# Optimization experiments

Measured on AMD Instinct MI355X. Metric: run time of the kernel, lower is better.

Reference implementation:

```python
import jax, jax.numpy as jnp
import numpy as np

B, D, DOUT, R, H = 16384, 1024, 1024, 8, 16
DH = D // 2  # route hidden dim


def setup_inputs() -> dict:
    key = jax.random.key(0)
    ks = jax.random.split(key, 12)
    s = 0.02
    return {
        "x": jax.random.normal(ks[0], (B, D), dtype=jnp.float32),
        # nn.MultiheadAttention packed in_proj: [3D, D] (q,k,v stacked)
        "in_proj_w": jax.random.normal(ks[1], (3 * D, D), dtype=jnp.float32) * s,
        "in_proj_b": jax.random.normal(ks[2], (3 * D,), dtype=jnp.float32) * s,
        "out_proj_w": jax.random.normal(ks[3], (D, D), dtype=jnp.float32) * s,
        "out_proj_b": jax.random.normal(ks[4], (D,), dtype=jnp.float32) * s,
        # R expert MLPs, batched: Linear(D, D//2) -> ReLU -> Linear(D//2, DOUT)
        "W1": jax.random.normal(ks[5], (R, DH, D), dtype=jnp.float32) * s,
        "b1": jax.random.normal(ks[6], (R, DH), dtype=jnp.float32) * s,
        "W2": jax.random.normal(ks[7], (R, DOUT, DH), dtype=jnp.float32) * s,
        "b2": jax.random.normal(ks[8], (R, DOUT), dtype=jnp.float32) * s,
        # gate: Linear(D, R) + softmax
        "Wg": jax.random.normal(ks[9], (R, D), dtype=jnp.float32) * s,
        "bg": jax.random.normal(ks[10], (R,), dtype=jnp.float32) * s,
    }


def reference(x, in_proj_w, in_proj_b, out_proj_w, out_proj_b, W1, b1, W2, b2, Wg, bg):
    # --- MultiheadAttention over seq_len == 1 ---
    # softmax over a single key position is exactly 1 (for every head),
    # so attn_output == V; the Q/K projections provably do not affect the
    # output or any gradient (d softmax(single logit) = 0). Hence only the
    # V slice of the packed in_proj and the output projection matter.
    Wv = in_proj_w[2 * D:]          # [D, D]
    bv = in_proj_b[2 * D:]          # [D]
    v = x @ Wv.T + bv               # [B, D]
    attended = v @ out_proj_w.T + out_proj_b  # [B, D]

    # --- R small expert MLPs as one batched/grouped GEMM (dropout in eval mode = identity) ---
    h = jax.nn.relu(jnp.einsum('bd,rhd->brh', attended, W1) + b1)   # [B, R, DH]
    route_out = jnp.einsum('brh,roh->bro', h, W2) + b2              # [B, R, DOUT]

    # --- softmax gate over routes, computed from the ORIGINAL x ---
    gate = jax.nn.softmax(x @ Wg.T + bg, axis=-1)                   # [B, R]

    # gate-weighted sum over routes
    return jnp.einsum('bro,br->bo', route_out, gate)                # [B, DOUT]
```

## Files before the change

kernel.cpp:

```cpp
#include <hip/hip_runtime.h>
#include <hip/hip_bf16.h>
#include <cstdint>

typedef __hip_bfloat16 bf16;
typedef __attribute__((ext_vector_type(8))) short bfrag;
typedef __attribute__((ext_vector_type(4))) float facc;

#define B_    16384
#define D_    1024
#define DOUT_ 1024
#define R_    8
#define DH_   512
#define RH_   4096

#define BM 256
#define BN 256
#define BK 64

#define NXCD 8

#define AS1(p) ((const __attribute__((address_space(1))) void*)(p))
#define AS3(p) ((__attribute__((address_space(3))) void*)(p))

#define DSR(dst, addr, off) \
    asm volatile("ds_read_b128 %0, %1 offset:%c2" : "=v"(dst) : "v"(addr), "i"(off))
#define LGKM(n) do { asm volatile("s_waitcnt lgkmcnt(" #n ")" ::: "memory"); \
                     __builtin_amdgcn_sched_barrier(0); } while (0)

static __device__ __forceinline__ uint32_t pack2bf(float a, float b) {
    unsigned short ua = __builtin_bit_cast(unsigned short, __float2bfloat16(a));
    unsigned short ub = __builtin_bit_cast(unsigned short, __float2bfloat16(b));
    return (uint32_t)ua | ((uint32_t)ub << 16);
}

__global__ void k_cvt(const float* __restrict__ in, bf16* __restrict__ out, long n)
{
    long i = ((long)blockIdx.x * blockDim.x + threadIdx.x) * 4;
    if (i >= n) return;
    float4 v = *reinterpret_cast<const float4*>(in + i);
    uint2 o;
    o.x = pack2bf(v.x, v.y);
    o.y = pack2bf(v.z, v.w);
    *reinterpret_cast<uint2*>(out + i) = o;
}

__global__ void k_cvt_w2(const float* __restrict__ W2, bf16* __restrict__ out)
{
    int b = blockIdx.x;
    int r = b >> 10;
    int o = b & 1023;
    const float4* src = reinterpret_cast<const float4*>(W2 + ((long)r * DOUT_ + o) * DH_);
    bf16* dst = out + (long)o * RH_ + r * DH_;
    int t = threadIdx.x;
    float4 v = src[t];
    uint2 p;
    p.x = pack2bf(v.x, v.y);
    p.y = pack2bf(v.z, v.w);
    *reinterpret_cast<uint2*>(dst + t * 4) = p;
}

__global__ __launch_bounds__(256) void k_cvt_wvT(const float* __restrict__ Wv,
                                                 bf16* __restrict__ outT)
{
    __shared__ float tile[64][65];
    const int j0 = blockIdx.y * 64;
    const int d0 = blockIdx.x * 64;
    const int tx = threadIdx.x & 15;
    const int ty = threadIdx.x >> 4;
    #pragma unroll
    for (int p = 0; p < 4; ++p) {
        int r = p * 16 + ty;
        float4 v = *reinterpret_cast<const float4*>(&Wv[(long)(j0 + r) * D_ + d0 + tx * 4]);
        tile[r][tx * 4 + 0] = v.x; tile[r][tx * 4 + 1] = v.y;
        tile[r][tx * 4 + 2] = v.z; tile[r][tx * 4 + 3] = v.w;
    }
    __syncthreads();
    #pragma unroll
    for (int p = 0; p < 4; ++p) {
        int r = p * 16 + ty;
        uint2 o;
        o.x = pack2bf(tile[tx * 4 + 0][r], tile[tx * 4 + 1][r]);
        o.y = pack2bf(tile[tx * 4 + 2][r], tile[tx * 4 + 3][r]);
        *reinterpret_cast<uint2*>(&outT[(long)(d0 + r) * D_ + j0 + tx * 4]) = o;
    }
}

__global__ __launch_bounds__(256) void k_beff(const float* __restrict__ Wout,
                                              const float* __restrict__ bv,
                                              const float* __restrict__ bout,
                                              float* __restrict__ beff)
{
    const int o = blockIdx.x;
    float s = 0.f;
    for (int d = threadIdx.x; d < D_; d += 256)
        s += Wout[(long)o * D_ + d] * bv[d];
    #pragma unroll
    for (int off = 32; off > 0; off >>= 1) s += __shfl_xor(s, off);
    __shared__ float ps[4];
    if ((threadIdx.x & 63) == 0) ps[threadIdx.x >> 6] = s;
    __syncthreads();
    if (threadIdx.x == 0)
        beff[o] = ps[0] + ps[1] + ps[2] + ps[3] + bout[o];
}

__global__ __launch_bounds__(256) void k_gate(const float* __restrict__ x,
                                              const float* __restrict__ Wg,
                                              const float* __restrict__ bg,
                                              float* __restrict__ gate)
{
    __shared__ float sWg[R_ * D_];
    __shared__ float sbg[R_];
    for (int i = threadIdx.x; i < R_ * D_ / 4; i += 256)
        reinterpret_cast<float4*>(sWg)[i] = reinterpret_cast<const float4*>(Wg)[i];
    if (threadIdx.x < R_) sbg[threadIdx.x] = bg[threadIdx.x];
    __syncthreads();

    const int lane = threadIdx.x & 63;
    const int wave = threadIdx.x >> 6;
    const int row  = blockIdx.x * 4 + wave;

    const float4* xr = reinterpret_cast<const float4*>(x + (long)row * D_);
    float s[R_] = {};
    #pragma unroll
    for (int c = 0; c < 4; ++c) {
        float4 xv = xr[lane + c * 64];
        #pragma unroll
        for (int r = 0; r < R_; ++r) {
            float4 wv = reinterpret_cast<const float4*>(sWg + r * D_)[lane + c * 64];
            s[r] += xv.x * wv.x + xv.y * wv.y + xv.z * wv.z + xv.w * wv.w;
        }
    }
    #pragma unroll
    for (int r = 0; r < R_; ++r) {
        float v = s[r];
        #pragma unroll
        for (int off = 32; off > 0; off >>= 1) v += __shfl_xor(v, off);
        s[r] = v + sbg[r];
    }
    float m = s[0];
    #pragma unroll
    for (int r = 1; r < R_; ++r) m = fmaxf(m, s[r]);
    float den = 0.f;
    #pragma unroll
    for (int r = 0; r < R_; ++r) { s[r] = __expf(s[r] - m); den += s[r]; }
    float inv = 1.f / den;
    if (lane < R_) gate[(long)row * R_ + lane] = s[lane] * inv;
}

#define MFMA_BF16 __builtin_amdgcn_mfma_f32_16x16x32_bf16

template <int EPI>
__global__ __launch_bounds__(512, 2)
void k_gemm(const bf16* __restrict__ A, const bf16* __restrict__ Bm,
            const float* __restrict__ bias, const float* __restrict__ gate,
            const float* __restrict__ b2v, void* __restrict__ Cout,
            int M, int N, int K, int gate_row0)
{
    __shared__ char lds[131072];

    const int tid  = threadIdx.x;
    const int lane = tid & 63;
    const int wave = tid >> 6;
    const int wr   = wave >> 2;
    const int wc   = wave & 3;

    const int nwg  = gridDim.x * gridDim.y;
    const int orig = blockIdx.y * gridDim.x + blockIdx.x;
    const int xcd  = orig % NXCD;
    const int q    = nwg / NXCD;
    const int rr   = nwg % NXCD;
    const int wgid = (xcd < rr ? xcd * (q + 1) : rr * (q + 1) + (xcd - rr) * q)
                   + orig / NXCD;
    const int bn0  = (wgid % gridDim.x) * BN;
    const int bm0  = (wgid / gridDim.x) * BM;

    const int lrow = lane & 15;
    const int kgrp = lane >> 4;

    const int s_colb  = ((tid & 7) * 16) ^ (((tid >> 3) & 7) << 4);
    const int s_row   = tid >> 3;
    const int lds_off = tid * 16;

    const long Kb   = (long)K * 2;
    const long r64  = 64 * Kb;
    const long r128 = 128 * Kb;
    const char* gA0 = (const char*)A  + (long)(bm0 + s_row) * Kb + s_colb;
    const char* gB0 = (const char*)Bm + (long)(bn0 + s_row) * Kb + s_colb;

    auto stageH = [&](int buf, int h, long kb) {
        char* ldst = lds + buf * 65536
                   + (h < 2 ? h * 16384 : 32768 + (h - 2) * 16384) + lds_off;
        const char* g = (h < 2 ? gA0 + h * r128 : gB0 + (h - 2) * r128) + kb;
        __builtin_amdgcn_global_load_lds(AS1(g),       AS3(ldst),        16, 0, 0);
        __builtin_amdgcn_global_load_lds(AS1(g + r64), AS3(ldst + 8192), 16, 0, 0);
    };

    const int swzk  = (lrow & 7) << 4;
    const int colK0 = (kgrp * 16) ^ swzk;
    const int colK1 = (kgrp * 16 + 64) ^ swzk;
    const uint32_t ldsbase = (uint32_t)(uintptr_t)AS3(lds);
    const uint32_t aA00 = ldsbase + (wr * 128 + lrow) * 128 + colK0;
    const uint32_t aA01 = ldsbase + (wr * 128 + lrow) * 128 + colK1;
    const uint32_t aB00 = ldsbase + 32768 + (wc * 64 + lrow) * 128 + colK0;
    const uint32_t aB01 = ldsbase + 32768 + (wc * 64 + lrow) * 128 + colK1;
    const uint32_t aA10 = aA00 + 65536, aA11 = aA01 + 65536;
    const uint32_t aB10 = aB00 + 65536, aB11 = aB01 + 65536;

    facc acc[8][4];
    #pragma unroll
    for (int m = 0; m < 8; ++m)
        #pragma unroll
        for (int n = 0; n < 4; ++n)
            acc[m][n] = facc{0.f, 0.f, 0.f, 0.f};

    const int NT = K / BK;

    bfrag aF[4][2];
    bfrag bHi[2][2];
    bfrag bLoE[2][2];
    bfrag bLoO[2][2];

    auto rdQ0 = [&](bfrag (&bLo)[2][2], uint32_t A0, uint32_t A1,
                    uint32_t B0, uint32_t B1) {
        DSR(bLo[0][0], B0, 0);    DSR(bLo[0][1], B1, 0);
        DSR(bLo[1][0], B0, 2048); DSR(bLo[1][1], B1, 2048);
        #pragma unroll
        for (int m = 0; m < 4; ++m) {
            DSR(aF[m][0], A0, m * 2048);
            DSR(aF[m][1], A1, m * 2048);
        }
    };

    stageH(0, 0, 0); stageH(0, 1, 0); stageH(0, 2, 0); stageH(0, 3, 0);
    stageH(1, 0, 128); stageH(1, 1, 128);
    asm volatile("s_waitcnt vmcnt(4)" ::: "memory");
    __builtin_amdgcn_s_barrier();
    rdQ0(bLoE, aA00, aA01, aB00, aB01);

    auto ktile = [&](int t, int curbuf,
                     uint32_t A0c, uint32_t A1c, uint32_t B0c, uint32_t B1c,
                     uint32_t A0n, uint32_t A1n, uint32_t B0n, uint32_t B1n,
                     bfrag (&bLoC)[2][2], bfrag (&bLoN)[2][2]) {
        const long k1b = (long)(t + 1) * 128;
        const long k2b = (long)(t + 2) * 128;
        const int  nb  = curbuf ^ 1;

        if (t + 1 < NT) stageH(nb, 2, k1b);
        __builtin_amdgcn_s_barrier();
        __builtin_amdgcn_s_setprio(1);
        LGKM(6);
        acc[0][0] = MFMA_BF16(aF[0][0], bLoC[0][0], acc[0][0], 0, 0, 0);
        acc[0][0] = MFMA_BF16(aF[0][1], bLoC[0][1], acc[0][0], 0, 0, 0);
        acc[0][1] = MFMA_BF16(aF[0][0], bLoC[1][0], acc[0][1], 0, 0, 0);
        acc[0][1] = MFMA_BF16(aF[0][1], bLoC[1][1], acc[0][1], 0, 0, 0);
        LGKM(4);
        acc[1][0] = MFMA_BF16(aF[1][0], bLoC[0][0], acc[1][0], 0, 0, 0);
        acc[1][0] = MFMA_BF16(aF[1][1], bLoC[0][1], acc[1][0], 0, 0, 0);
        acc[1][1] = MFMA_BF16(aF[1][0], bLoC[1][0], acc[1][1], 0, 0, 0);
        acc[1][1] = MFMA_BF16(aF[1][1], bLoC[1][1], acc[1][1], 0, 0, 0);
        LGKM(2);
        acc[2][0] = MFMA_BF16(aF[2][0], bLoC[0][0], acc[2][0], 0, 0, 0);
        acc[2][0] = MFMA_BF16(aF[2][1], bLoC[0][1], acc[2][0], 0, 0, 0);
        acc[2][1] = MFMA_BF16(aF[2][0], bLoC[1][0], acc[2][1], 0, 0, 0);
        acc[2][1] = MFMA_BF16(aF[2][1], bLoC[1][1], acc[2][1], 0, 0, 0);
        LGKM(0);
        acc[3][0] = MFMA_BF16(aF[3][0], bLoC[0][0], acc[3][0], 0, 0, 0);
        acc[3][0] = MFMA_BF16(aF[3][1], bLoC[0][1], acc[3][0], 0, 0, 0);
        acc[3][1] = MFMA_BF16(aF[3][0], bLoC[1][0], acc[3][1], 0, 0, 0);
        acc[3][1] = MFMA_BF16(aF[3][1], bLoC[1][1], acc[3][1], 0, 0, 0);
        __builtin_amdgcn_s_setprio(0);
        DSR(bHi[0][0], B0c, 2 * 2048); DSR(bHi[0][1], B1c, 2 * 2048);
        DSR(bHi[1][0], B0c, 3 * 2048); DSR(bHi[1][1], B1c, 3 * 2048);
        __builtin_amdgcn_s_barrier();

        if (t + 1 < NT) stageH(nb, 3, k1b);
        __builtin_amdgcn_s_barrier();
        __builtin_amdgcn_s_setprio(1);
        LGKM(2);
        #pragma unroll
        for (int m = 0; m < 4; ++m) {
            acc[m][2] = MFMA_BF16(aF[m][0], bHi[0][0], acc[m][2], 0, 0, 0);
            acc[m][2] = MFMA_BF16(aF[m][1], bHi[0][1], acc[m][2], 0, 0, 0);
        }
        LGKM(0);
        #pragma unroll
        for (int m = 0; m < 4; ++m) {
            acc[m][3] = MFMA_BF16(aF[m][0], bHi[1][0], acc[m][3], 0, 0, 0);
            acc[m][3] = MFMA_BF16(aF[m][1], bHi[1][1], acc[m][3], 0, 0, 0);
        }
        __builtin_amdgcn_s_setprio(0);
        #pragma unroll
        for (int m = 0; m < 4; ++m) {
            DSR(aF[m][0], A0c, (4 + m) * 2048);
            DSR(aF[m][1], A1c, (4 + m) * 2048);
        }
        __builtin_amdgcn_s_barrier();

        if (t + 2 < NT) stageH(curbuf, 0, k2b);
        __builtin_amdgcn_s_barrier();
        __builtin_amdgcn_s_setprio(1);
        LGKM(6);
        acc[4][2] = MFMA_BF16(aF[0][0], bHi[0][0], acc[4][2], 0, 0, 0);
        acc[4][2] = MFMA_BF16(aF[0][1], bHi[0][1], acc[4][2], 0, 0, 0);
        acc[4][3] = MFMA_BF16(aF[0][0], bHi[1][0], acc[4][3], 0, 0, 0);
        acc[4][3] = MFMA_BF16(aF[0][1], bHi[1][1], acc[4][3], 0, 0, 0);
        LGKM(4);
        acc[5][2] = MFMA_BF16(aF[1][0], bHi[0][0], acc[5][2], 0, 0, 0);
        acc[5][2] = MFMA_BF16(aF[1][1], bHi[0][1], acc[5][2], 0, 0, 0);
        acc[5][3] = MFMA_BF16(aF[1][0], bHi[1][0], acc[5][3], 0, 0, 0);
        acc[5][3] = MFMA_BF16(aF[1][1], bHi[1][1], acc[5][3], 0, 0, 0);
        LGKM(2);
        acc[6][2] = MFMA_BF16(aF[2][0], bHi[0][0], acc[6][2], 0, 0, 0);
        acc[6][2] = MFMA_BF16(aF[2][1], bHi[0][1], acc[6][2], 0, 0, 0);
        acc[6][3] = MFMA_BF16(aF[2][0], bHi[1][0], acc[6][3], 0, 0, 0);
        acc[6][3] = MFMA_BF16(aF[2][1], bHi[1][1], acc[6][3], 0, 0, 0);
        LGKM(0);
        acc[7][2] = MFMA_BF16(aF[3][0], bHi[0][0], acc[7][2], 0, 0, 0);
        acc[7][2] = MFMA_BF16(aF[3][1], bHi[0][1], acc[7][2], 0, 0, 0);
        acc[7][3] = MFMA_BF16(aF[3][0], bHi[1][0], acc[7][3], 0, 0, 0);
        acc[7][3] = MFMA_BF16(aF[3][1], bHi[1][1], acc[7][3], 0, 0, 0);
        __builtin_amdgcn_s_setprio(0);
        __builtin_amdgcn_s_barrier();

        if (t + 2 < NT) {
            stageH(curbuf, 1, k2b);
            asm volatile("s_waitcnt vmcnt(4)" ::: "memory");
        } else if (t + 1 < NT) {
            asm volatile("s_waitcnt vmcnt(0)" ::: "memory");
        }
        __builtin_amdgcn_s_barrier();
        __builtin_amdgcn_s_setprio(1);
        #pragma unroll
        for (int m = 0; m < 4; ++m) {
            acc[4 + m][0] = MFMA_BF16(aF[m][0], bLoC[0][0], acc[4 + m][0], 0, 0, 0);
            acc[4 + m][0] = MFMA_BF16(aF[m][1], bLoC[0][1], acc[4 + m][0], 0, 0, 0);
            acc[4 + m][1] = MFMA_BF16(aF[m][0], bLoC[1][0], acc[4 + m][1], 0, 0, 0);
            acc[4 + m][1] = MFMA_BF16(aF[m][1], bLoC[1][1], acc[4 + m][1], 0, 0, 0);
        }
        __builtin_amdgcn_s_setprio(0);
        if (t + 1 < NT) rdQ0(bLoN, A0n, A1n, B0n, B1n);
        __builtin_amdgcn_s_barrier();
    };

    for (int t = 0; t < NT; t += 2) {
        ktile(t,     0, aA00, aA01, aB00, aB01, aA10, aA11, aB10, aB11, bLoE, bLoO);
        ktile(t + 1, 1, aA10, aA11, aB10, aB11, aA00, aA01, aB00, aB01, bLoO, bLoE);
    }

    if constexpr (EPI == 2) {
        float* Cf = reinterpret_cast<float*>(Cout);
        float b2c[4][R_];
        #pragma unroll
        for (int n = 0; n < 4; ++n) {
            const int col = bn0 + wc * 64 + n * 16 + lrow;
            #pragma unroll
            for (int r = 0; r < R_; ++r) b2c[n][r] = b2v[r * N + col];
        }
        #pragma unroll
        for (int m = 0; m < 8; ++m) {
            #pragma unroll
            for (int j = 0; j < 4; ++j) {
                const int row = bm0 + wr * 128 + m * 16 + kgrp * 4 + j;
                const float* g = gate + (long)(gate_row0 + row) * R_;
                float gv[R_];
                #pragma unroll
                for (int r = 0; r < R_; ++r) gv[r] = g[r];
                #pragma unroll
                for (int n = 0; n < 4; ++n) {
                    const int col = bn0 + wc * 64 + n * 16 + lrow;
                    float sv = acc[m][n][j];
                    #pragma unroll
                    for (int r = 0; r < R_; ++r) sv += gv[r] * b2c[n][r];
                    Cf[(long)row * N + col] = sv;
                }
            }
        }
    } else {
        bf16* Cb = reinterpret_cast<bf16*>(Cout);
        float bcol[4];
        #pragma unroll
        for (int n = 0; n < 4; ++n) {
            if constexpr (EPI == 3) bcol[n] = 0.f;
            else bcol[n] = bias[bn0 + wc * 64 + n * 16 + lrow];
        }
        #pragma unroll
        for (int m = 0; m < 8; ++m) {
            #pragma unroll
            for (int j = 0; j < 4; ++j) {
                const int row = bm0 + wr * 128 + m * 16 + kgrp * 4 + j;
                float gv[4];
                if constexpr (EPI == 1) {
                    #pragma unroll
                    for (int n = 0; n < 4; ++n) {
                        const int col = bn0 + wc * 64 + n * 16 + lrow;
                        gv[n] = gate[(long)(gate_row0 + row) * R_ + (col >> 9)];
                    }
                }
                #pragma unroll
                for (int n = 0; n < 4; ++n) {
                    const int col = bn0 + wc * 64 + n * 16 + lrow;
                    float v = acc[m][n][j] + bcol[n];
                    if constexpr (EPI == 1) v = fmaxf(v, 0.f) * gv[n];
                    Cb[(long)row * N + col] = __float2bfloat16(v);
                }
            }
        }
    }
}

extern "C" void kernel_launch(void* const* d_in, const int* in_sizes, int n_in,
                              void* d_out, int out_size, void* d_ws, size_t ws_size,
                              hipStream_t stream)
{
    const float* x   = (const float*)d_in[0];
    const float* ipw = (const float*)d_in[1];
    const float* ipb = (const float*)d_in[2];
    const float* opw = (const float*)d_in[3];
    const float* opb = (const float*)d_in[4];
    const float* W1  = (const float*)d_in[5];
    const float* b1  = (const float*)d_in[6];
    const float* W2  = (const float*)d_in[7];
    const float* b2  = (const float*)d_in[8];
    const float* Wg  = (const float*)d_in[9];
    const float* bg  = (const float*)d_in[10];
    float* out = (float*)d_out;

    const float* Wv_f = ipw + (size_t)2 * D_ * D_;
    const float* bv_f = ipb + 2 * D_;

    char* ws = (char*)d_ws;
    size_t off = 0;
    auto alloc = [&](size_t bytes) -> void* {
        void* p = ws + off;
        off += (bytes + 255) & ~(size_t)255;
        return p;
    };

    bf16* xb   = (bf16*)alloc((size_t)B_ * D_ * 2);
    bf16* ab   = (bf16*)alloc((size_t)B_ * D_ * 2);
    bf16* Wob  = (bf16*)alloc((size_t)D_ * D_ * 2);
    bf16* WvT  = (bf16*)alloc((size_t)D_ * D_ * 2);
    bf16* Weff = (bf16*)alloc((size_t)D_ * D_ * 2);
    float* beff = (float*)alloc((size_t)D_ * 4);
    bf16* W1b  = (bf16*)alloc((size_t)RH_ * D_ * 2);
    bf16* W2b  = (bf16*)alloc((size_t)DOUT_ * RH_ * 2);
    float* gate = (float*)alloc((size_t)B_ * R_ * 4);

    int mc = B_;
    while (off + (size_t)mc * RH_ * 2 > ws_size && mc > 1024) mc >>= 1;
    bf16* hb = (bf16*)alloc((size_t)mc * RH_ * 2);

    k_cvt<<<(B_ * D_) / 1024, 256, 0, stream>>>(x, xb, (long)B_ * D_);
    k_cvt<<<(D_ * D_) / 1024, 256, 0, stream>>>(opw, Wob, (long)D_ * D_);
    k_cvt_wvT<<<dim3(16, 16), 256, 0, stream>>>(Wv_f, WvT);
    k_cvt<<<(RH_ * D_) / 1024, 256, 0, stream>>>(W1, W1b, (long)RH_ * D_);
    k_cvt_w2<<<R_ * DOUT_, 128, 0, stream>>>(W2, W2b);
    k_beff<<<D_, 256, 0, stream>>>(opw, bv_f, opb, beff);

    k_gate<<<B_ / 4, 256, 0, stream>>>(x, Wg, bg, gate);

    k_gemm<3><<<dim3(D_ / BN, D_ / BM), 512, 0, stream>>>(
        Wob, WvT, nullptr, nullptr, nullptr, Weff, D_, D_, D_, 0);

    k_gemm<0><<<dim3(D_ / BN, B_ / BM), 512, 0, stream>>>(
        xb, Weff, beff, nullptr, nullptr, ab, B_, D_, D_, 0);

    for (int m0 = 0; m0 < B_; m0 += mc) {
        k_gemm<1><<<dim3(RH_ / BN, mc / BM), 512, 0, stream>>>(
            ab + (size_t)m0 * D_, W1b, b1, gate, nullptr, hb, mc, RH_, D_, m0);
        k_gemm<2><<<dim3(DOUT_ / BN, mc / BM), 512, 0, stream>>>(
            hb, W2b, nullptr, gate, b2, out + (size_t)m0 * DOUT_, mc, DOUT_, RH_, m0);
    }
}
```

Before: 381.8 us.

## Split-K the weight-fusion GEMM and restructure k-tile prefetch staging

The Wout·Wv fusion GEMM only launches 16 workgroups on a 1024x1024 output, so it is split four ways along K into fp32 partial buffers, and a new reduction kernel sums them and converts the result to bf16. Separately, the GEMM main loop now issues the next tile's B halves together two phases ahead instead of one tile ahead, which changes prefetch depth and vmcnt waits for every GEMM launch. This adds an extra kernel launch and 16 MB of fp32 partial traffic, and the altered staging schedule touches the dominant large GEMMs.

```diff
diff --git a/kernel.cpp b/kernel.cpp
--- a/kernel.cpp
+++ b/kernel.cpp
@@ -18,6 +18,7 @@
 #define BK 64
 
 #define NXCD 8
+#define KSPLIT 4
 
 #define AS1(p) ((const __attribute__((address_space(1))) void*)(p))
 #define AS3(p) ((__attribute__((address_space(3))) void*)(p))
@@ -103,6 +104,21 @@
         beff[o] = ps[0] + ps[1] + ps[2] + ps[3] + bout[o];
 }
 
+__global__ __launch_bounds__(256) void k_wred(const float* __restrict__ part,
+                                              bf16* __restrict__ out)
+{
+    const long n = (long)D_ * D_;
+    long i = ((long)blockIdx.x * 256 + threadIdx.x) * 4;
+    float4 a = *reinterpret_cast<const float4*>(part + i);
+    float4 b = *reinterpret_cast<const float4*>(part + n + i);
+    float4 c = *reinterpret_cast<const float4*>(part + 2 * n + i);
+    float4 d = *reinterpret_cast<const float4*>(part + 3 * n + i);
+    uint2 o;
+    o.x = pack2bf(a.x + b.x + c.x + d.x, a.y + b.y + c.y + d.y);
+    o.y = pack2bf(a.z + b.z + c.z + d.z, a.w + b.w + c.w + d.w);
+    *reinterpret_cast<uint2*>(out + i) = o;
+}
+
 __global__ __launch_bounds__(256) void k_gate(const float* __restrict__ x,
                                               const float* __restrict__ Wg,
                                               const float* __restrict__ bg,
@@ -154,7 +170,7 @@
 void k_gemm(const bf16* __restrict__ A, const bf16* __restrict__ Bm,
             const float* __restrict__ bias, const float* __restrict__ gate,
             const float* __restrict__ b2v, void* __restrict__ Cout,
-            int M, int N, int K, int gate_row0)
+            int M, int N, int K, int gate_row0, int ldk)
 {
     __shared__ char lds[131072];
 
@@ -181,11 +197,12 @@
     const int s_row   = tid >> 3;
     const int lds_off = tid * 16;
 
-    const long Kb   = (long)K * 2;
+    const long Kb   = (long)ldk * 2;
+    const long zoff = (long)blockIdx.z * K * 2;
     const long r64  = 64 * Kb;
     const long r128 = 128 * Kb;
-    const char* gA0 = (const char*)A  + (long)(bm0 + s_row) * Kb + s_colb;
-    const char* gB0 = (const char*)Bm + (long)(bn0 + s_row) * Kb + s_colb;
+    const char* gA0 = (const char*)A  + (long)(bm0 + s_row) * Kb + s_colb + zoff;
+    const char* gB0 = (const char*)Bm + (long)(bn0 + s_row) * Kb + s_colb + zoff;
 
     auto stageH = [&](int buf, int h, long kb) {
         char* ldst = lds + buf * 65536
@@ -231,9 +248,9 @@
         }
     };
 
-    stageH(0, 0, 0); stageH(0, 1, 0); stageH(0, 2, 0); stageH(0, 3, 0);
-    stageH(1, 0, 128); stageH(1, 1, 128);
-    asm volatile("s_waitcnt vmcnt(4)" ::: "memory");
+    stageH(0, 0, 0);   stageH(0, 1, 0);   stageH(0, 2, 0);   stageH(0, 3, 0);
+    stageH(1, 0, 128); stageH(1, 1, 128); stageH(1, 2, 128); stageH(1, 3, 128);
+    asm volatile("s_waitcnt vmcnt(8)" ::: "memory");
     __builtin_amdgcn_s_barrier();
     rdQ0(bLoE, aA00, aA01, aB00, aB01);
 
@@ -241,11 +258,8 @@
                      uint32_t A0c, uint32_t A1c, uint32_t B0c, uint32_t B1c,
                      uint32_t A0n, uint32_t A1n, uint32_t B0n, uint32_t B1n,
                      bfrag (&bLoC)[2][2], bfrag (&bLoN)[2][2]) {
-        const long k1b = (long)(t + 1) * 128;
         const long k2b = (long)(t + 2) * 128;
-        const int  nb  = curbuf ^ 1;
-
-        if (t + 1 < NT) stageH(nb, 2, k1b);
+
         __builtin_amdgcn_s_barrier();
         __builtin_amdgcn_s_setprio(1);
         LGKM(6);
@@ -273,7 +287,6 @@
         DSR(bHi[1][0], B0c, 3 * 2048); DSR(bHi[1][1], B1c, 3 * 2048);
         __builtin_amdgcn_s_barrier();
 
-        if (t + 1 < NT) stageH(nb, 3, k1b);
         __builtin_amdgcn_s_barrier();
         __builtin_amdgcn_s_setprio(1);
         LGKM(2);
@@ -296,7 +309,7 @@
         }
         __builtin_amdgcn_s_barrier();
 
-        if (t + 2 < NT) stageH(curbuf, 0, k2b);
+        if (t + 2 < NT) { stageH(curbuf, 2, k2b); stageH(curbuf, 3, k2b); }
         __builtin_amdgcn_s_barrier();
         __builtin_amdgcn_s_setprio(1);
         LGKM(6);
@@ -323,8 +336,8 @@
         __builtin_amdgcn_s_barrier();
 
         if (t + 2 < NT) {
-            stageH(curbuf, 1, k2b);
-            asm volatile("s_waitcnt vmcnt(4)" ::: "memory");
+            stageH(curbuf, 0, k2b); stageH(curbuf, 1, k2b);
+            asm volatile("s_waitcnt vmcnt(8)" ::: "memory");
         } else if (t + 1 < NT) {
             asm volatile("s_waitcnt vmcnt(0)" ::: "memory");
         }
@@ -375,14 +388,25 @@
                 }
             }
         }
+    } else if constexpr (EPI == 4) {
+        float* Cf = reinterpret_cast<float*>(Cout) + (size_t)blockIdx.z * M * N;
+        #pragma unroll
+        for (int m = 0; m < 8; ++m) {
+            #pragma unroll
+            for (int j = 0; j < 4; ++j) {
+                const int row = bm0 + wr * 128 + m * 16 + kgrp * 4 + j;
+                #pragma unroll
+                for (int n = 0; n < 4; ++n) {
+                    const int col = bn0 + wc * 64 + n * 16 + lrow;
+                    Cf[(long)row * N + col] = acc[m][n][j];
+                }
+            }
+        }
     } else {
         bf16* Cb = reinterpret_cast<bf16*>(Cout);
         float bcol[4];
         #pragma unroll
-        for (int n = 0; n < 4; ++n) {
-            if constexpr (EPI == 3) bcol[n] = 0.f;
-            else bcol[n] = bias[bn0 + wc * 64 + n * 16 + lrow];
-        }
+        for (int n = 0; n < 4; ++n) bcol[n] = bias[bn0 + wc * 64 + n * 16 + lrow];
         #pragma unroll
         for (int m = 0; m < 8; ++m) {
             #pragma unroll
@@ -441,6 +465,7 @@
     bf16* Wob  = (bf16*)alloc((size_t)D_ * D_ * 2);
     bf16* WvT  = (bf16*)alloc((size_t)D_ * D_ * 2);
     bf16* Weff = (bf16*)alloc((size_t)D_ * D_ * 2);
+    float* Wpart = (float*)alloc((size_t)KSPLIT * D_ * D_ * 4);
     float* beff = (float*)alloc((size_t)D_ * 4);
     bf16* W1b  = (bf16*)alloc((size_t)RH_ * D_ * 2);
     bf16* W2b  = (bf16*)alloc((size_t)DOUT_ * RH_ * 2);
@@ -459,16 +484,17 @@
 
     k_gate<<<B_ / 4, 256, 0, stream>>>(x, Wg, bg, gate);
 
-    k_gemm<3><<<dim3(D_ / BN, D_ / BM), 512, 0, stream>>>(
-        Wob, WvT, nullptr, nullptr, nullptr, Weff, D_, D_, D_, 0);
+    k_gemm<4><<<dim3(D_ / BN, D_ / BM, KSPLIT), 512, 0, stream>>>(
+        Wob, WvT, nullptr, nullptr, nullptr, Wpart, D_, D_, D_ / KSPLIT, 0, D_);
+    k_wred<<<(D_ * D_) / 1024, 256, 0, stream>>>(Wpart, Weff);
 
     k_gemm<0><<<dim3(D_ / BN, B_ / BM), 512, 0, stream>>>(
-        xb, Weff, beff, nullptr, nullptr, ab, B_, D_, D_, 0);
+        xb, Weff, beff, nullptr, nullptr, ab, B_, D_, D_, 0, D_);
 
     for (int m0 = 0; m0 < B_; m0 += mc) {
         k_gemm<1><<<dim3(RH_ / BN, mc / BM), 512, 0, stream>>>(
-            ab + (size_t)m0 * D_, W1b, b1, gate, nullptr, hb, mc, RH_, D_, m0);
+            ab + (size_t)m0 * D_, W1b, b1, gate, nullptr, hb, mc, RH_, D_, m0, D_);
         k_gemm<2><<<dim3(DOUT_ / BN, mc / BM), 512, 0, stream>>>(
-            hb, W2b, nullptr, gate, b2, out + (size_t)m0 * DOUT_, mc, DOUT_, RH_, m0);
-    }
-}
+            hb, W2b, nullptr, gate, b2, out + (size_t)m0 * DOUT_, mc, DOUT_, RH_, m0, RH_);
+    }
+}
```

After: 377.5 us. No clear change (-1.1%).
